# Kernel optimization log

Measured on AMD Instinct MI355X. Metric: run time of the kernel, lower is better.

Reference implementation:

```python
import jax, jax.numpy as jnp
import numpy as np
from jax import lax

BOS = 0
B, T, U = 8, 256, 64
IN, ENC_H, DEC_H, P, J, V = 80, 512, 512, 512, 512, 1024


def lstm_layer(x, Wih, Whh, b):
    """PyTorch-style LSTM layer. x: [B,T,I]; Wih: [4H,I]; Whh: [4H,H]; b: [4H]."""
    Bn = x.shape[0]
    H = Whh.shape[1]
    xp = jnp.einsum('bti,gi->btg', x, Wih) + b  # precompute input projections [B,T,4H]
    h0 = jnp.zeros((Bn, H), x.dtype)

    def step(carry, xt):
        h, c = carry
        g = xt + h @ Whh.T
        i, f, gg, o = jnp.split(g, 4, axis=-1)
        c = jax.nn.sigmoid(f) * c + jax.nn.sigmoid(i) * jnp.tanh(gg)
        h = jax.nn.sigmoid(o) * jnp.tanh(c)
        return (h, c), h

    _, hs = lax.scan(step, (h0, h0), xp.transpose(1, 0, 2))
    return hs.transpose(1, 0, 2)  # [B,T,H]


def setup_inputs() -> dict:
    key = jax.random.key(0)
    ks = jax.random.split(key, 20)
    s = 0.04  # ~1/sqrt(H) init scale
    inp = {
        'xs': jax.random.normal(ks[0], (B, T, IN), jnp.float32),
        'ys': jax.random.randint(ks[1], (B, U), 0, V),
        # encoder LSTM layer 0 / 1
        'enc_Wih0': jax.random.normal(ks[2], (4 * ENC_H, IN), jnp.float32) * s,
        'enc_Whh0': jax.random.normal(ks[3], (4 * ENC_H, ENC_H), jnp.float32) * s,
        'enc_b0': jnp.zeros((4 * ENC_H,), jnp.float32),
        'enc_Wih1': jax.random.normal(ks[4], (4 * ENC_H, ENC_H), jnp.float32) * s,
        'enc_Whh1': jax.random.normal(ks[5], (4 * ENC_H, ENC_H), jnp.float32) * s,
        'enc_b1': jnp.zeros((4 * ENC_H,), jnp.float32),
        'enc_projW': jax.random.normal(ks[6], (P, ENC_H), jnp.float32) * s,
        'enc_projb': jnp.zeros((P,), jnp.float32),
        # decoder
        'embed': jax.random.normal(ks[7], (V, DEC_H), jnp.float32) * s,
        'dec_Wih': jax.random.normal(ks[8], (4 * DEC_H, DEC_H), jnp.float32) * s,
        'dec_Whh': jax.random.normal(ks[9], (4 * DEC_H, DEC_H), jnp.float32) * s,
        'dec_b': jnp.zeros((4 * DEC_H,), jnp.float32),
        'dec_projW': jax.random.normal(ks[10], (P, DEC_H), jnp.float32) * s,
        'dec_projb': jnp.zeros((P,), jnp.float32),
        # joint MLP: Linear(2P -> J), Tanh, Linear(J -> V)
        'jW1': jax.random.normal(ks[11], (J, 2 * P), jnp.float32) * s,
        'jb1': jnp.zeros((J,), jnp.float32),
        'jW2': jax.random.normal(ks[12], (V, J), jnp.float32) * s,
        'jb2': jnp.zeros((V,), jnp.float32),
    }
    return inp


def reference(xs, ys, enc_Wih0, enc_Whh0, enc_b0, enc_Wih1, enc_Whh1, enc_b1,
              enc_projW, enc_projb, embed, dec_Wih, dec_Whh, dec_b,
              dec_projW, dec_projb, jW1, jb1, jW2, jb2):
    # Encoder: 2-layer LSTM + projection
    h = lstm_layer(xs, enc_Wih0, enc_Whh0, enc_b0)
    h = lstm_layer(h, enc_Wih1, enc_Whh1, enc_b1)
    h_enc = h @ enc_projW.T + enc_projb  # [B,T,P]

    # Decoder: BOS pad, embed, 1-layer LSTM + projection
    ys_p = jnp.pad(ys, ((0, 0), (1, 0)), constant_values=BOS)  # [B,U+1]
    e = embed[ys_p]
    hd = lstm_layer(e, dec_Wih, dec_Whh, dec_b)
    h_dec = hd @ dec_projW.T + dec_projb  # [B,U+1,P]

    # Joint: cat([h_enc,h_dec]) @ W1.T == h_enc @ W1[:,:P].T + h_dec @ W1[:,P:].T
    pre_enc = jnp.einsum('btp,jp->btj', h_enc, jW1[:, :P])
    pre_dec = jnp.einsum('bup,jp->buj', h_dec, jW1[:, P:])
    z = jnp.tanh(pre_enc[:, :, None, :] + pre_dec[:, None, :, :] + jb1)  # [B,T,U+1,J]
    logits = jnp.einsum('btuj,vj->btuv', z, jW2) + jb2  # [B,T,U+1,V]
    return logits
```

## Files before the change

### kernel.cpp

```cpp
#include <hip/hip_runtime.h>


typedef _Float16 f16;
typedef _Float16 f16x8 __attribute__((ext_vector_type(8)));
typedef float f32x4 __attribute__((ext_vector_type(4)));
using u32 = unsigned int;

#define BB   8
#define TT   256
#define UU1  65
#define HH   512
#define G4   2048
#define PP   512
#define JJ   512
#define VV   1024
#define SENT 0xFFFFFFFFu

#define LOADX(p)     __hip_atomic_load((p), __ATOMIC_RELAXED, __HIP_MEMORY_SCOPE_AGENT)
#define STOREX(p, v) __hip_atomic_store((p), (v), __ATOMIC_RELAXED, __HIP_MEMORY_SCOPE_AGENT)

static __device__ __forceinline__ u32 packf16(float a, float b) {
  f16 ha = (f16)a, hb = (f16)b;
  unsigned short ua = __builtin_bit_cast(unsigned short, ha);
  unsigned short ub = __builtin_bit_cast(unsigned short, hb);
  return (u32)ua | ((u32)ub << 16);
}
static __device__ __forceinline__ float sigm(float x) {
  x = fminf(30.f, fmaxf(-30.f, x));
  return __builtin_amdgcn_rcpf(1.f + __expf(-x));
}
static __device__ __forceinline__ float ftanh(float x) {
  x = fminf(15.f, fmaxf(-15.f, x));
  float t = __expf(2.f * x);
  return (t - 1.f) * __builtin_amdgcn_rcpf(t + 1.f);
}

__global__ void k_init(u32* __restrict__ p, int n, int z1, int z2) {
  int i = blockIdx.x * 256 + threadIdx.x;
  if (i >= n) return;
  bool z = (i < 2048) | ((u32)(i - z1) < 2048u) | ((u32)(i - z2) < 2048u);
  p[i] = z ? 0u : SENT;
}

struct CastSeg { const float* s; f16* d; int n4; };
struct CastArgs { CastSeg seg[10]; };
__global__ void k_cast_all(CastArgs a, int total4) {
  int i = blockIdx.x * 256 + threadIdx.x;
  if (i >= total4) return;
  int k = 0, off = i;
  while (off >= a.seg[k].n4) { off -= a.seg[k].n4; ++k; }
  const float4 v = *(const float4*)(a.seg[k].s + (size_t)off * 4);
  uint2 p; p.x = packf16(v.x, v.y); p.y = packf16(v.z, v.w);
  *(uint2*)(a.seg[k].d + (size_t)off * 4) = p;
}

__global__ void k_embed(const int* __restrict__ ys, const float* __restrict__ emb,
                        float* __restrict__ e) {
  int row = blockIdx.x;
  int b = row / UU1, u = row % UU1;
  int idx = (u == 0) ? 0 : ys[b * (UU1 - 1) + (u - 1)];
  const float4* s = (const float4*)(emb + (size_t)idx * HH);
  float4* d = (float4*)(e + (size_t)row * HH);
  d[threadIdx.x] = s[threadIdx.x];
}

__global__ void k_biasdot(const float* __restrict__ jW1, const float* __restrict__ encPb,
                          const float* __restrict__ dPb, const float* __restrict__ jb1,
                          float* __restrict__ bce, float* __restrict__ bcd) {
  int j = blockIdx.x * 256 + threadIdx.x;
  if (j >= 512) return;
  const float* rowE = jW1 + (size_t)j * 1024;
  const float* rowD = rowE + 512;
  float s1 = 0.f, s2 = 0.f;
  for (int p = 0; p < 512; p += 4) {
    float4 a = *(const float4*)(rowE + p), b = *(const float4*)(encPb + p);
    s1 += a.x * b.x + a.y * b.y + a.z * b.z + a.w * b.w;
    float4 c = *(const float4*)(rowD + p), d = *(const float4*)(dPb + p);
    s2 += c.x * d.x + c.y * d.y + c.z * d.z + c.w * d.w;
  }
  bce[j] = s1; bcd[j] = s2 + jb1[j];
}

__global__ __launch_bounds__(256) void k_gemm(
    const float* __restrict__ A, const f16* __restrict__ B,
    const float* __restrict__ bias, float* __restrict__ C,
    int M, int N, int K, int lda, int ldb) {
  __shared__ f16 As[128][72];
  __shared__ f16 Bs[128][72];
  int tid = threadIdx.x;
  int mb = blockIdx.y * 128, nb = blockIdx.x * 128;
  int wave = tid >> 6, lane = tid & 63;
  int wm = wave >> 1, wn = wave & 1;
  int rowa = lane & 15, kg = lane >> 4;
  f32x4 acc[4][4] = {};
  for (int k0 = 0; k0 < K; k0 += 64) {
    for (int idx = tid; idx < 2048; idx += 256) {
      int r = idx >> 4, cq = idx & 15;
      int gm = mb + r, gk = k0 + cq * 4;
      float4 v = make_float4(0.f, 0.f, 0.f, 0.f);
      if (gm < M && gk + 3 < K) v = *(const float4*)(A + (size_t)gm * lda + gk);
      uint2 p; p.x = packf16(v.x, v.y); p.y = packf16(v.z, v.w);
      *(uint2*)&As[r][cq * 4] = p;
    }
    for (int idx = tid; idx < 1024; idx += 256) {
      int r = idx >> 3, c8 = idx & 7;
      int gn = nb + r, gk = k0 + c8 * 8;
      uint4 v = make_uint4(0u, 0u, 0u, 0u);
      if (gn < N && gk + 7 < K) v = *(const uint4*)(B + (size_t)gn * ldb + gk);
      *(uint4*)&Bs[r][c8 * 8] = v;
    }
    __syncthreads();
#pragma unroll
    for (int kf = 0; kf < 2; ++kf) {
      f16x8 af[4], bf[4];
#pragma unroll
      for (int mt = 0; mt < 4; ++mt)
        af[mt] = *(const f16x8*)&As[wm * 64 + mt * 16 + rowa][kf * 32 + kg * 8];
#pragma unroll
      for (int nt = 0; nt < 4; ++nt)
        bf[nt] = *(const f16x8*)&Bs[wn * 64 + nt * 16 + rowa][kf * 32 + kg * 8];
#pragma unroll
      for (int mt = 0; mt < 4; ++mt)
#pragma unroll
        for (int nt = 0; nt < 4; ++nt)
          acc[mt][nt] = __builtin_amdgcn_mfma_f32_16x16x32_f16(af[mt], bf[nt], acc[mt][nt], 0, 0, 0);
    }
    __syncthreads();
  }
#pragma unroll
  for (int nt = 0; nt < 4; ++nt) {
    int gn = nb + wn * 64 + nt * 16 + rowa;
    float bv = bias ? bias[gn] : 0.f;
#pragma unroll
    for (int mt = 0; mt < 4; ++mt)
#pragma unroll
      for (int r = 0; r < 4; ++r) {
        int gm = mb + wm * 64 + mt * 16 + kg * 4 + r;
        if (gm < M) C[(size_t)gm * N + gn] = acc[mt][nt][r] + bv;
      }
  }
}

__global__ __launch_bounds__(256) void k_gemmT(
    const float* __restrict__ A, int lda, const f16* __restrict__ B2,
    f16* __restrict__ C16) {
  __shared__ f16 As[128][72];
  __shared__ f16 Bs[128][72];
  int tid = threadIdx.x;
  int mb = blockIdx.y * 128, nb = blockIdx.x * 128;
  int wave = tid >> 6, lane = tid & 63;
  int wm = wave >> 1, wn = wave & 1;
  int rowa = lane & 15, kg = lane >> 4;
  f32x4 acc[4][4] = {};
  for (int k0 = 0; k0 < 512; k0 += 64) {
    for (int idx = tid; idx < 2048; idx += 256) {
      int r = idx >> 4, cq = idx & 15;
      float4 v = *(const float4*)(A + (size_t)(mb + r) * lda + k0 + cq * 4);
      uint2 p; p.x = packf16(v.x, v.y); p.y = packf16(v.z, v.w);
      *(uint2*)&As[r][cq * 4] = p;
    }
    for (int idx = tid; idx < 1024; idx += 256) {
      int r = idx >> 4, c8 = idx & 15;
      uint4 v = *(const uint4*)(B2 + (size_t)(k0 + r) * 512 + nb + c8 * 8);
      f16 tmp[8]; *(uint4*)tmp = v;
#pragma unroll
      for (int e = 0; e < 8; ++e) Bs[c8 * 8 + e][r] = tmp[e];
    }
    __syncthreads();
#pragma unroll
    for (int kf = 0; kf < 2; ++kf) {
      f16x8 af[4], bf[4];
#pragma unroll
      for (int mt = 0; mt < 4; ++mt)
        af[mt] = *(const f16x8*)&As[wm * 64 + mt * 16 + rowa][kf * 32 + kg * 8];
#pragma unroll
      for (int nt = 0; nt < 4; ++nt)
        bf[nt] = *(const f16x8*)&Bs[wn * 64 + nt * 16 + rowa][kf * 32 + kg * 8];
#pragma unroll
      for (int mt = 0; mt < 4; ++mt)
#pragma unroll
        for (int nt = 0; nt < 4; ++nt)
          acc[mt][nt] = __builtin_amdgcn_mfma_f32_16x16x32_f16(af[mt], bf[nt], acc[mt][nt], 0, 0, 0);
    }
    __syncthreads();
  }
#pragma unroll
  for (int nt = 0; nt < 4; ++nt) {
    int gn = nb + wn * 64 + nt * 16 + rowa;
#pragma unroll
    for (int mt = 0; mt < 4; ++mt)
#pragma unroll
      for (int r = 0; r < 4; ++r) {
        int gm = mb + wm * 64 + mt * 16 + kg * 4 + r;
        C16[(size_t)gm * 512 + gn] = (f16)acc[mt][nt][r];
      }
  }
}

template <int NW>
static __device__ __forceinline__ void poll_batch(const u32* const* p, u32* vv) {
#pragma unroll
  for (int k = 0; k < NW; ++k) vv[k] = LOADX(p[k]);
  int gd = 0;
  while (++gd < (1 << 18)) {
    bool any = false;
#pragma unroll
    for (int k = 0; k < NW; ++k) any = any | (vv[k] == SENT);
    if (!any) break;
    __builtin_amdgcn_s_sleep(4);
#pragma unroll
    for (int k = 0; k < NW; ++k)
      if (vv[k] == SENT) vv[k] = LOADX(p[k]);
  }
}
static __device__ __forceinline__ void guard_spin(const u32* gp) {
  u32 v = LOADX(gp);
  int gd = 0;
  while (v == SENT && ++gd < (1 << 18)) {
    __builtin_amdgcn_s_sleep(1);
    v = LOADX(gp);
  }
}

static __device__ __forceinline__ void lstm_16(
    int wg, const float* __restrict__ xp, const f16* __restrict__ Whh,
    u32* __restrict__ hseq,
    float* __restrict__ hs, int S) {
  extern __shared__ char smem[];
  f16 (*W)[520] = (f16(*)[520])smem;
  f16 (*H)[520] = (f16(*)[520])(smem + 133120);
  float (*gat)[8][36] = (float(*)[8][36])(smem + 133120 + 8320);
  const int tid = threadIdx.x;
  const int u0 = wg * 32;
  const int wave = tid >> 6, lane = tid & 63;
  const int rowa = lane & 15, kg = lane >> 4;
  const int b = lane >> 3, ju = lane & 7;
  const int uglob = u0 + wave * 8 + ju;

  for (int idx = tid; idx < 128 * 64; idx += 256) {
    int r = idx >> 6, ck = idx & 63;
    int w = r >> 5, g = (r >> 3) & 3, u = r & 7;
    uint4 v = *(const uint4*)(Whh + ((size_t)(g * 512 + u0 + w * 8 + u)) * 512 + ck * 8);
    *(uint4*)&W[r][ck * 8] = v;
  }
  __syncthreads();

  float c = 0.f;
  for (int t = 0; t < S; ++t) {
    const u32* hb = hseq + (size_t)t * 2048;
    if (tid < 16) guard_spin(hb + tid * 16);
    __syncthreads();

    size_t xpo = ((size_t)b * S + t) * (size_t)G4 + uglob;
    float xi = xp[xpo], xf = xp[xpo + 512], xg = xp[xpo + 1024], xo = xp[xpo + 1536];

    const u32* ptr[8];
    u32 vv[8];
#pragma unroll
    for (int k = 0; k < 8; ++k) ptr[k] = hb + ((tid + k * 256) >> 8) * 256 + ((tid + k * 256) & 255);
    poll_batch<8>(ptr, vv);
#pragma unroll
    for (int k = 0; k < 8; ++k) {
      int idx = tid + k * 256;
      ((u32*)H)[(idx >> 8) * 260 + (idx & 255)] = vv[k];
    }
    __syncthreads();

    f32x4 acc0 = {0.f, 0.f, 0.f, 0.f}, acc1 = {0.f, 0.f, 0.f, 0.f};
#pragma unroll
    for (int kf = 0; kf < 16; ++kf) {
      f16x8 af = {};
      if (rowa < 8) af = *(const f16x8*)&H[rowa][kf * 32 + kg * 8];
      f16x8 b0 = *(const f16x8*)&W[wave * 32 + rowa][kf * 32 + kg * 8];
      f16x8 b1 = *(const f16x8*)&W[wave * 32 + 16 + rowa][kf * 32 + kg * 8];
      acc0 = __builtin_amdgcn_mfma_f32_16x16x32_f16(af, b0, acc0, 0, 0, 0);
      acc1 = __builtin_amdgcn_mfma_f32_16x16x32_f16(af, b1, acc1, 0, 0, 0);
    }
    if (kg < 2) {
#pragma unroll
      for (int r = 0; r < 4; ++r) {
        gat[wave][kg * 4 + r][rowa] = acc0[r];
        gat[wave][kg * 4 + r][16 + rowa] = acc1[r];
      }
    }
    float gi = gat[wave][b][ju] + xi;
    float gf = gat[wave][b][8 + ju] + xf;
    float gg = gat[wave][b][16 + ju] + xg;
    float go = gat[wave][b][24 + ju] + xo;
    c = sigm(gf) * c + sigm(gi) * ftanh(gg);
    float h = sigm(go) * ftanh(c);

    float hn = __shfl_down(h, 1);
    if ((ju & 1) == 0)
      STOREX(hseq + (size_t)(t + 1) * 2048 + ((b * 512 + uglob) >> 1), packf16(h, hn));
    if (hs) hs[((size_t)b * S + t) * HH + uglob] = h;
  }
}

static __device__ __forceinline__ void lstm_l1(
    int wg, const float* __restrict__ gb, const f16* __restrict__ Wih,
    const f16* __restrict__ Whh, const u32* __restrict__ hin,
    u32* __restrict__ hseq, float* __restrict__ hs, int S) {
  extern __shared__ char smem[];
  f16 (*W)[1032] = (f16(*)[1032])smem;
  f16 (*H)[1032] = (f16(*)[1032])(smem + 132096);
  float (*gat)[8][20] = (float(*)[8][20])(smem + 132096 + 16512);
  const int tid = threadIdx.x;
  const int u0 = wg * 16;
  const int wave = tid >> 6, lane = tid & 63;
  const int rowa = lane & 15, kg = lane >> 4;
  const int b = lane >> 2, ju = lane & 3;
  const int uglob = u0 + wave * 4 + ju;

  for (int idx = tid; idx < 64 * 64; idx += 256) {
    int r = idx >> 6, ck = idx & 63;
    int w = r >> 4, g = (r >> 2) & 3, u = r & 3;
    size_t grow = (size_t)(g * 512 + u0 + w * 4 + u) * 512;
    *(uint4*)&W[r][ck * 8]       = *(const uint4*)(Whh + grow + ck * 8);
    *(uint4*)&W[r][512 + ck * 8] = *(const uint4*)(Wih + grow + ck * 8);
  }
  float gbi = 0.f, gbf = 0.f, gbg = 0.f, gbo = 0.f;
  if (lane < 32) {
    gbi = gb[uglob]; gbf = gb[512 + uglob];
    gbg = gb[1024 + uglob]; gbo = gb[1536 + uglob];
  }
  __syncthreads();

  float c = 0.f;
  for (int t = 0; t < S; ++t) {
    const u32* hbS = hseq + (size_t)t * 2048;
    const u32* hbU = hin + (size_t)(t + 1) * 2048;
    if (tid < 32)       guard_spin(hbS + tid * 8);
    else if (tid < 48)  guard_spin(hbU + (tid - 32) * 16);
    __syncthreads();
    const u32* ptr[16];
    u32 vv[16];
#pragma unroll
    for (int k = 0; k < 8; ++k) {
      int idx = tid + k * 256;
      int r = idx >> 8, cu = idx & 255;
      ptr[k] = hbS + r * 256 + cu;
      ptr[k + 8] = hbU + r * 256 + cu;
    }
    poll_batch<16>(ptr, vv);
#pragma unroll
    for (int k = 0; k < 8; ++k) {
      int idx = tid + k * 256;
      int r = idx >> 8, cu = idx & 255;
      ((u32*)H)[r * 516 + cu] = vv[k];
      ((u32*)H)[r * 516 + 256 + cu] = vv[k + 8];
    }
    __syncthreads();

    f32x4 accA = {0.f, 0.f, 0.f, 0.f}, accB = {0.f, 0.f, 0.f, 0.f};
#pragma unroll
    for (int kf = 0; kf < 16; ++kf) {
      f16x8 afA = {}, afB = {};
      if (rowa < 8) {
        afA = *(const f16x8*)&H[rowa][kf * 32 + kg * 8];
        afB = *(const f16x8*)&H[rowa][(kf + 16) * 32 + kg * 8];
      }
      f16x8 bfA = *(const f16x8*)&W[wave * 16 + rowa][kf * 32 + kg * 8];
      f16x8 bfB = *(const f16x8*)&W[wave * 16 + rowa][(kf + 16) * 32 + kg * 8];
      accA = __builtin_amdgcn_mfma_f32_16x16x32_f16(afA, bfA, accA, 0, 0, 0);
      accB = __builtin_amdgcn_mfma_f32_16x16x32_f16(afB, bfB, accB, 0, 0, 0);
    }
    if (kg < 2) {
#pragma unroll
      for (int r = 0; r < 4; ++r) gat[wave][kg * 4 + r][rowa] = accA[r] + accB[r];
    }
    if (lane < 32) {
      float gi = gat[wave][b][ju]      + gbi;
      float gf = gat[wave][b][4 + ju]  + gbf;
      float gg = gat[wave][b][8 + ju]  + gbg;
      float go = gat[wave][b][12 + ju] + gbo;
      c = sigm(gf) * c + sigm(gi) * ftanh(gg);
      float h = sigm(go) * ftanh(c);
      float hn = __shfl_down(h, 1);
      if ((ju & 1) == 0)
        STOREX(hseq + (size_t)(t + 1) * 2048 + (b * 256 + (uglob >> 1)), packf16(h, hn));
      hs[((size_t)b * S + t) * HH + uglob] = h;
    }
  }
}

__global__ __launch_bounds__(256, 1) void k_lstm3(
    const float* xp0, const f16* Whh0, u32* hseq0,
    const float* b1, const f16* Wih1, const f16* Whh1, u32* hseq1, float* h1s,
    const float* xpd, const f16* Whhd, u32* hseqD, float* hds) {
  int g = blockIdx.x;
  if (g < 16)      lstm_16(g, xp0, Whh0, hseq0, nullptr, TT);
  else if (g < 48) lstm_l1(g - 16, b1, Wih1, Whh1, hseq0, hseq1, h1s, TT);
  else             lstm_16(g - 48, xpd, Whhd, hseqD, hds, UU1);
}

__global__ __launch_bounds__(512, 6) void k_joint(
    const float* __restrict__ pre_enc,
    const float* __restrict__ pre_dec,
    const f16* __restrict__ jW2,
    const float* __restrict__ jb2,
    float* __restrict__ out) {
  __shared__ f16 Z[32][520];
  __shared__ f16 Bs[64][72];
  __shared__ float Cs[32][68];
  int tid = threadIdx.x;
  int m0 = blockIdx.x * 32;
  const int wave = tid >> 6, lane = tid & 63;
  const int mt = wave >> 2, vt = wave & 3;
  const int rowa = lane & 15, kg = lane >> 4;
  const int r8 = tid >> 3, c8 = tid & 7;

  uint4 nreg = *(const uint4*)(jW2 + (size_t)r8 * JJ + c8 * 8);

  {
    int r = tid >> 4, q = tid & 15;
    int m = m0 + r;
    int bb = m / (TT * UU1);
    int rem = m % (TT * UU1);
    int t = rem / UU1, u = rem % UU1;
    const float* pe = pre_enc + ((size_t)bb * TT + t) * JJ + q * 32;
    const float* pd = pre_dec + ((size_t)bb * UU1 + u) * JJ + q * 32;
    for (int i = 0; i < 32; i += 8) {
      float4 e0 = *(const float4*)(pe + i);
      float4 e1 = *(const float4*)(pe + i + 4);
      float4 d0 = *(const float4*)(pd + i);
      float4 d1 = *(const float4*)(pd + i + 4);
      float z0 = ftanh(e0.x + d0.x), z1 = ftanh(e0.y + d0.y);
      float z2 = ftanh(e0.z + d0.z), z3 = ftanh(e0.w + d0.w);
      float z4 = ftanh(e1.x + d1.x), z5 = ftanh(e1.y + d1.y);
      float z6 = ftanh(e1.z + d1.z), z7 = ftanh(e1.w + d1.w);
      uint4 p; p.x = packf16(z0, z1); p.y = packf16(z2, z3);
      p.z = packf16(z4, z5); p.w = packf16(z6, z7);
      *(uint4*)&Z[r][q * 32 + i] = p;
    }
  }

  f32x4 acc = {};
  for (int it = 0; it < 128; ++it) {
    const int vc = it >> 3, ks = it & 7;
    __syncthreads();
    *(uint4*)&Bs[r8][c8 * 8] = nreg;
    if (it < 127) {
      int nvc = (it + 1) >> 3, nks = (it + 1) & 7;
      nreg = *(const uint4*)(jW2 + (size_t)(nvc * 64 + r8) * JJ + nks * 64 + c8 * 8);
    }
    __syncthreads();
#pragma unroll
    for (int kf = 0; kf < 2; ++kf) {
      f16x8 af = *(const f16x8*)&Bs[vt * 16 + rowa][kf * 32 + kg * 8];
      f16x8 bf = *(const f16x8*)&Z[mt * 16 + rowa][ks * 64 + kf * 32 + kg * 8];
      acc = __builtin_amdgcn_mfma_f32_16x16x32_f16(af, bf, acc, 0, 0, 0);
    }
    if (ks == 7) {
      int vl = vt * 16 + kg * 4;
      float4 bv = *(const float4*)(jb2 + vc * 64 + vl);
      f32x4 st;
      st[0] = acc[0] + bv.x; st[1] = acc[1] + bv.y;
      st[2] = acc[2] + bv.z; st[3] = acc[3] + bv.w;
      *(f32x4*)&Cs[mt * 16 + rowa][vl] = st;
      acc = (f32x4){0.f, 0.f, 0.f, 0.f};
      __syncthreads();
      int m = tid >> 4, vi = (tid & 15) * 4;
      f32x4 row = *(const f32x4*)&Cs[m][vi];
      __builtin_nontemporal_store(row,
          (f32x4*)(out + (size_t)(m0 + m) * VV + vc * 64 + vi));
    }
  }
}

extern "C" void kernel_launch(void* const* d_in, const int* in_sizes, int n_in,
                              void* d_out, int out_size, void* d_ws, size_t ws_size,
                              hipStream_t stream) {
  const float* xs    = (const float*)d_in[0];
  const int*   ys    = (const int*)d_in[1];
  const float* Wih0  = (const float*)d_in[2];
  const float* Whh0  = (const float*)d_in[3];
  const float* b0    = (const float*)d_in[4];
  const float* Wih1  = (const float*)d_in[5];
  const float* Whh1  = (const float*)d_in[6];
  const float* b1    = (const float*)d_in[7];
  const float* encPW = (const float*)d_in[8];
  const float* encPb = (const float*)d_in[9];
  const float* embed = (const float*)d_in[10];
  const float* dWih  = (const float*)d_in[11];
  const float* dWhh  = (const float*)d_in[12];
  const float* db    = (const float*)d_in[13];
  const float* dPW   = (const float*)d_in[14];
  const float* dPb   = (const float*)d_in[15];
  const float* jW1   = (const float*)d_in[16];
  const float* jb1   = (const float*)d_in[17];
  const float* jW2   = (const float*)d_in[18];
  const float* jb2   = (const float*)d_in[19];
  float* out = (float*)d_out;

  char* base = (char*)d_ws;
  size_t off = 0;
  auto alc = [&](size_t bytes) -> char* {
    char* p = base + off;
    off = (off + bytes + 255) & ~(size_t)255;
    return p;
  };
  f16* Wih0h = (f16*)alc((size_t)2048 * 80 * 2);
  f16* Whh0h = (f16*)alc((size_t)2048 * 512 * 2);
  f16* Wih1h = (f16*)alc((size_t)2048 * 512 * 2);
  f16* Whh1h = (f16*)alc((size_t)2048 * 512 * 2);
  f16* dWihh = (f16*)alc((size_t)2048 * 512 * 2);
  f16* dWhhh = (f16*)alc((size_t)2048 * 512 * 2);
  f16* ePWh  = (f16*)alc((size_t)512 * 512 * 2);
  f16* dPWh  = (f16*)alc((size_t)512 * 512 * 2);
  f16* jW2h  = (f16*)alc((size_t)1024 * 512 * 2);
  f16* Wceh  = (f16*)alc((size_t)512 * 512 * 2);
  f16* Wcdh  = (f16*)alc((size_t)512 * 512 * 2);
  float* bce  = (float*)alc((size_t)512 * 4);
  float* bcd  = (float*)alc((size_t)512 * 4);
  float* e    = (float*)alc((size_t)520 * 512 * 4);
  float* xp0  = (float*)alc((size_t)2048 * 2048 * 4);
  float* xpd  = (float*)alc((size_t)520 * 2048 * 4);
  float* h1s  = (float*)alc((size_t)2048 * 512 * 4);
  float* hds  = (float*)alc((size_t)520 * 512 * 4);
  float* penc = (float*)alc((size_t)2048 * 512 * 4);
  float* pdec = (float*)alc((size_t)520 * 512 * 4);
  u32* hseq0 = (u32*)alc((size_t)(TT + 1) * 2048 * 4);
  u32* hseq1 = (u32*)alc((size_t)(TT + 1) * 2048 * 4);
  u32* hseqD = (u32*)alc((size_t)(UU1 + 1) * 2048 * 4);
  if (off > ws_size) return;

  {
    int n = (int)(((TT + 1) * 2 + (UU1 + 1)) * 2048);
    int z1 = (int)(hseq1 - hseq0), z2 = (int)(hseqD - hseq0);
    k_init<<<dim3((n + 255) / 256), dim3(256), 0, stream>>>(hseq0, n, z1, z2);
  }
  {
    CastArgs ca = {};
    auto seg = [&](int i, const float* s, f16* d, size_t n) {
      ca.seg[i].s = s; ca.seg[i].d = d; ca.seg[i].n4 = (int)(n / 4);
    };
    seg(0, Wih0, Wih0h, (size_t)2048 * 80);
    seg(1, Whh0, Whh0h, (size_t)2048 * 512);
    seg(2, Wih1, Wih1h, (size_t)2048 * 512);
    seg(3, Whh1, Whh1h, (size_t)2048 * 512);
    seg(4, dWih, dWihh, (size_t)2048 * 512);
    seg(5, dWhh, dWhhh, (size_t)2048 * 512);
    seg(6, encPW, ePWh, (size_t)512 * 512);
    seg(7, dPW, dPWh, (size_t)512 * 512);
    seg(8, jW2, jW2h, (size_t)1024 * 512);
    int total4 = 0;
    for (int i = 0; i < 9; ++i) total4 += ca.seg[i].n4;
    k_cast_all<<<dim3((total4 + 255) / 256), dim3(256), 0, stream>>>(ca, total4);
  }
  k_gemmT<<<dim3(4, 4), dim3(256), 0, stream>>>(jW1, 1024, ePWh, Wceh);
  k_gemmT<<<dim3(4, 4), dim3(256), 0, stream>>>(jW1 + 512, 1024, dPWh, Wcdh);
  k_biasdot<<<dim3(2), dim3(256), 0, stream>>>(jW1, encPb, dPb, jb1, bce, bcd);

  k_embed<<<dim3(520), dim3(128), 0, stream>>>(ys, embed, e);

  auto gemm = [&](const float* A, const f16* B, const float* bias, float* C,
                  int M, int N, int K, int lda, int ldb) {
    k_gemm<<<dim3(N / 128, (M + 127) / 128), dim3(256), 0, stream>>>(
        A, B, bias, C, M, N, K, lda, ldb);
  };

  gemm(xs, Wih0h, b0, xp0, 2048, 2048, 80, 80, 80);
  gemm(e, dWihh, db, xpd, 520, 2048, 512, 512, 512);

  k_lstm3<<<dim3(64), dim3(256), 151168, stream>>>(
      xp0, Whh0h, hseq0,
      b1, Wih1h, Whh1h, hseq1, h1s,
      xpd, dWhhh, hseqD, hds);

  gemm(h1s, Wceh, bce, penc, 2048, 512, 512, 512, 512);
  gemm(hds, Wcdh, bcd, pdec, 520, 512, 512, 512, 512);

  k_joint<<<dim3(4160), dim3(512), 0, stream>>>(penc, pdec, jW2h, jb2, out);
}
```

Baseline: 1.428 ms.

## Fuse projections and joint into persistent LSTM kernel with flag-based streaming

```diff
diff --git a/kernel.cpp b/kernel.cpp
--- a/kernel.cpp
+++ b/kernel.cpp
@@ -11,7 +11,6 @@
 #define UU1  65
 #define HH   512
 #define G4   2048
-#define PP   512
 #define JJ   512
 #define VV   1024
 #define SENT 0xFFFFFFFFu
@@ -224,8 +223,7 @@
 
 static __device__ __forceinline__ void lstm_16(
     int wg, const float* __restrict__ xp, const f16* __restrict__ Whh,
-    u32* __restrict__ hseq,
-    float* __restrict__ hs, int S) {
+    u32* __restrict__ hseq, int S) {
   extern __shared__ char smem[];
   f16 (*W)[520] = (f16(*)[520])smem;
   f16 (*H)[520] = (f16(*)[520])(smem + 133120);
@@ -293,14 +291,13 @@
     float hn = __shfl_down(h, 1);
     if ((ju & 1) == 0)
       STOREX(hseq + (size_t)(t + 1) * 2048 + ((b * 512 + uglob) >> 1), packf16(h, hn));
-    if (hs) hs[((size_t)b * S + t) * HH + uglob] = h;
   }
 }
 
 static __device__ __forceinline__ void lstm_l1(
     int wg, const float* __restrict__ gb, const f16* __restrict__ Wih,
     const f16* __restrict__ Whh, const u32* __restrict__ hin,
-    u32* __restrict__ hseq, float* __restrict__ hs, int S) {
+    u32* __restrict__ hseq, int S) {
   extern __shared__ char smem[];
   f16 (*W)[1032] = (f16(*)[1032])smem;
   f16 (*H)[1032] = (f16(*)[1032])(smem + 132096);
@@ -379,93 +376,178 @@
       float hn = __shfl_down(h, 1);
       if ((ju & 1) == 0)
         STOREX(hseq + (size_t)(t + 1) * 2048 + (b * 256 + (uglob >> 1)), packf16(h, hn));
-      hs[((size_t)b * S + t) * HH + uglob] = h;
-    }
-  }
-}
-
-__global__ __launch_bounds__(256, 1) void k_lstm3(
-    const float* xp0, const f16* Whh0, u32* hseq0,
-    const float* b1, const f16* Wih1, const f16* Whh1, u32* hseq1, float* h1s,
-    const float* xpd, const f16* Whhd, u32* hseqD, float* hds) {
-  int g = blockIdx.x;
-  if (g < 16)      lstm_16(g, xp0, Whh0, hseq0, nullptr, TT);
-  else if (g < 48) lstm_l1(g - 16, b1, Wih1, Whh1, hseq0, hseq1, h1s, TT);
-  else             lstm_16(g - 48, xpd, Whhd, hseqD, hds, UU1);
-}
-
-__global__ __launch_bounds__(512, 6) void k_joint(
-    const float* __restrict__ pre_enc,
-    const float* __restrict__ pre_dec,
-    const f16* __restrict__ jW2,
-    const float* __restrict__ jb2,
+    }
+  }
+}
+
+static __device__ __forceinline__ void proj_prod(
+    int wg, const u32* __restrict__ hseq, const f16* __restrict__ Wc,
+    const float* __restrict__ bc, float* __restrict__ outS, int S,
+    int gs, int gc) {
+  extern __shared__ char smem[];
+  f16 (*W)[520] = (f16(*)[520])smem;
+  f16 (*H)[520] = (f16(*)[520])(smem + 66560);
+  const int tid = threadIdx.x;
+  const int wave = tid >> 6, lane = tid & 63;
+  const int rowa = lane & 15, kg = lane >> 4;
+  const int c0 = wg * 64;
+  const int j = c0 + wave * 16 + rowa;
+
+  for (int idx = tid; idx < 64 * 64; idx += 256) {
+    int r = idx >> 6, ck = idx & 63;
+    uint4 v = *(const uint4*)(Wc + (size_t)(c0 + r) * 512 + ck * 8);
+    *(uint4*)&W[r][ck * 8] = v;
+  }
+  for (int idx = tid; idx < 16 * 260; idx += 256) ((u32*)H)[idx] = 0u;
+  const float bj = bc[j];
+  __syncthreads();
+
+  for (int t = 0; t < S; ++t) {
+    const u32* hb = hseq + (size_t)(t + 1) * 2048;
+    if (tid < gc) guard_spin(hb + tid * gs);
+    __syncthreads();
+    const u32* ptr[8];
+    u32 vv[8];
+#pragma unroll
+    for (int k = 0; k < 8; ++k) ptr[k] = hb + ((tid + k * 256) >> 8) * 256 + ((tid + k * 256) & 255);
+    poll_batch<8>(ptr, vv);
+#pragma unroll
+    for (int k = 0; k < 8; ++k) {
+      int idx = tid + k * 256;
+      ((u32*)H)[(idx >> 8) * 260 + (idx & 255)] = vv[k];
+    }
+    __syncthreads();
+
+    f32x4 acc = {0.f, 0.f, 0.f, 0.f};
+#pragma unroll
+    for (int kf = 0; kf < 16; ++kf) {
+      f16x8 af = {};
+      if (rowa < 8) af = *(const f16x8*)&H[rowa][kf * 32 + kg * 8];
+      f16x8 bf = *(const f16x8*)&W[wave * 16 + rowa][kf * 32 + kg * 8];
+      acc = __builtin_amdgcn_mfma_f32_16x16x32_f16(af, bf, acc, 0, 0, 0);
+    }
+    if (kg < 2) {
+#pragma unroll
+      for (int r = 0; r < 4; ++r) {
+        float val = acc[r] + bj;
+        STOREX((u32*)(outS + ((size_t)t * 8 + kg * 4 + r) * 512 + j),
+               __builtin_bit_cast(u32, val));
+      }
+    }
+  }
+}
+
+static __device__ __forceinline__ void joint_tile(
+    int j, const float* __restrict__ pencS, const float* __restrict__ pdecS,
+    const f16* __restrict__ jW2, const float* __restrict__ jb2,
     float* __restrict__ out) {
-  __shared__ f16 Z[32][520];
-  __shared__ f16 Bs[64][72];
-  __shared__ float Cs[32][68];
-  int tid = threadIdx.x;
-  int m0 = blockIdx.x * 32;
+  extern __shared__ char smem[];
+  f16 (*Z)[520] = (f16(*)[520])smem;
+  f16 (*Bs)[72] = (f16(*)[72])(smem + 49920);
+  float (*Cs)[68] = (float(*)[68])(smem + 49920 + 9216);
+  const int tid = threadIdx.x;
+  const int t = j >> 4, b = (j >> 1) & 7, uh = j & 1;
+  const int u0 = uh * 32, nrow = uh ? 33 : 32;
+  const size_t mbase = (size_t)b * (TT * UU1) + (size_t)t * UU1 + u0;
   const int wave = tid >> 6, lane = tid & 63;
-  const int mt = wave >> 2, vt = wave & 3;
   const int rowa = lane & 15, kg = lane >> 4;
-  const int r8 = tid >> 3, c8 = tid & 7;
-
-  uint4 nreg = *(const uint4*)(jW2 + (size_t)r8 * JJ + c8 * 8);
-
+
+  const int rr = tid >> 2, cc = (tid & 3) * 16;
+  uint4 n0 = *(const uint4*)(jW2 + (size_t)rr * JJ + cc);
+  uint4 n1 = *(const uint4*)(jW2 + (size_t)rr * JJ + cc + 8);
+
+  for (int idx = tid; idx < 48 * 260; idx += 256) ((u32*)Z)[idx] = 0u;
   {
-    int r = tid >> 4, q = tid & 15;
-    int m = m0 + r;
-    int bb = m / (TT * UU1);
-    int rem = m % (TT * UU1);
-    int t = rem / UU1, u = rem % UU1;
-    const float* pe = pre_enc + ((size_t)bb * TT + t) * JJ + q * 32;
-    const float* pd = pre_dec + ((size_t)bb * UU1 + u) * JJ + q * 32;
-    for (int i = 0; i < 32; i += 8) {
-      float4 e0 = *(const float4*)(pe + i);
-      float4 e1 = *(const float4*)(pe + i + 4);
-      float4 d0 = *(const float4*)(pd + i);
-      float4 d1 = *(const float4*)(pd + i + 4);
-      float z0 = ftanh(e0.x + d0.x), z1 = ftanh(e0.y + d0.y);
-      float z2 = ftanh(e0.z + d0.z), z3 = ftanh(e0.w + d0.w);
-      float z4 = ftanh(e1.x + d1.x), z5 = ftanh(e1.y + d1.y);
-      float z6 = ftanh(e1.z + d1.z), z7 = ftanh(e1.w + d1.w);
-      uint4 p; p.x = packf16(z0, z1); p.y = packf16(z2, z3);
-      p.z = packf16(z4, z5); p.w = packf16(z6, z7);
-      *(uint4*)&Z[r][q * 32 + i] = p;
-    }
-  }
-
-  f32x4 acc = {};
+    const u32* pe = (const u32*)(pencS + ((size_t)t * 8 + b) * 512);
+    for (int r = tid >> 4; r < nrow; r += 16) {
+      const u32* pd = (const u32*)(pdecS + ((size_t)(u0 + r) * 8 + b) * 512);
+      int cbase = (tid & 15) * 32;
+      for (int c8 = 0; c8 < 4; ++c8) {
+        const u32* ptr[8];
+        u32 ve[8], vd[8];
+#pragma unroll
+        for (int k = 0; k < 8; ++k) ptr[k] = pe + cbase + c8 * 8 + k;
+        poll_batch<8>(ptr, ve);
+#pragma unroll
+        for (int k = 0; k < 8; ++k) ptr[k] = pd + cbase + c8 * 8 + k;
+        poll_batch<8>(ptr, vd);
+        uint4 p;
+        float z0 = ftanh(__builtin_bit_cast(float, ve[0]) + __builtin_bit_cast(float, vd[0]));
+        float z1 = ftanh(__builtin_bit_cast(float, ve[1]) + __builtin_bit_cast(float, vd[1]));
+        float z2 = ftanh(__builtin_bit_cast(float, ve[2]) + __builtin_bit_cast(float, vd[2]));
+        float z3 = ftanh(__builtin_bit_cast(float, ve[3]) + __builtin_bit_cast(float, vd[3]));
+        float z4 = ftanh(__builtin_bit_cast(float, ve[4]) + __builtin_bit_cast(float, vd[4]));
+        float z5 = ftanh(__builtin_bit_cast(float, ve[5]) + __builtin_bit_cast(float, vd[5]));
+        float z6 = ftanh(__builtin_bit_cast(float, ve[6]) + __builtin_bit_cast(float, vd[6]));
+        float z7 = ftanh(__builtin_bit_cast(float, ve[7]) + __builtin_bit_cast(float, vd[7]));
+        p.x = packf16(z0, z1); p.y = packf16(z2, z3);
+        p.z = packf16(z4, z5); p.w = packf16(z6, z7);
+        *(uint4*)&Z[r][cbase + c8 * 8] = p;
+      }
+    }
+  }
+
+  f32x4 acc[3] = {};
   for (int it = 0; it < 128; ++it) {
     const int vc = it >> 3, ks = it & 7;
     __syncthreads();
-    *(uint4*)&Bs[r8][c8 * 8] = nreg;
+    *(uint4*)&Bs[rr][cc] = n0;
+    *(uint4*)&Bs[rr][cc + 8] = n1;
     if (it < 127) {
       int nvc = (it + 1) >> 3, nks = (it + 1) & 7;
-      nreg = *(const uint4*)(jW2 + (size_t)(nvc * 64 + r8) * JJ + nks * 64 + c8 * 8);
+      const f16* p = jW2 + (size_t)(nvc * 64 + rr) * JJ + nks * 64 + cc;
+      n0 = *(const uint4*)p;
+      n1 = *(const uint4*)(p + 8);
     }
     __syncthreads();
 #pragma unroll
     for (int kf = 0; kf < 2; ++kf) {
-      f16x8 af = *(const f16x8*)&Bs[vt * 16 + rowa][kf * 32 + kg * 8];
-      f16x8 bf = *(const f16x8*)&Z[mt * 16 + rowa][ks * 64 + kf * 32 + kg * 8];
-      acc = __builtin_amdgcn_mfma_f32_16x16x32_f16(af, bf, acc, 0, 0, 0);
+      f16x8 af = *(const f16x8*)&Bs[wave * 16 + rowa][kf * 32 + kg * 8];
+#pragma unroll
+      for (int mt = 0; mt < 3; ++mt) {
+        f16x8 bf = *(const f16x8*)&Z[mt * 16 + rowa][ks * 64 + kf * 32 + kg * 8];
+        acc[mt] = __builtin_amdgcn_mfma_f32_16x16x32_f16(af, bf, acc[mt], 0, 0, 0);
+      }
     }
     if (ks == 7) {
-      int vl = vt * 16 + kg * 4;
+      int vl = wave * 16 + kg * 4;
       float4 bv = *(const float4*)(jb2 + vc * 64 + vl);
-      f32x4 st;
-      st[0] = acc[0] + bv.x; st[1] = acc[1] + bv.y;
-      st[2] = acc[2] + bv.z; st[3] = acc[3] + bv.w;
-      *(f32x4*)&Cs[mt * 16 + rowa][vl] = st;
-      acc = (f32x4){0.f, 0.f, 0.f, 0.f};
+#pragma unroll
+      for (int mt = 0; mt < 3; ++mt) {
+        int row = mt * 16 + rowa;
+        if (row < nrow) {
+          f32x4 st;
+          st[0] = acc[mt][0] + bv.x; st[1] = acc[mt][1] + bv.y;
+          st[2] = acc[mt][2] + bv.z; st[3] = acc[mt][3] + bv.w;
+          *(f32x4*)&Cs[row][vl] = st;
+        }
+        acc[mt] = (f32x4){0.f, 0.f, 0.f, 0.f};
+      }
       __syncthreads();
-      int m = tid >> 4, vi = (tid & 15) * 4;
-      f32x4 row = *(const f32x4*)&Cs[m][vi];
-      __builtin_nontemporal_store(row,
-          (f32x4*)(out + (size_t)(m0 + m) * VV + vc * 64 + vi));
-    }
-  }
+      for (int r = tid >> 4; r < nrow; r += 16) {
+        int vi = (tid & 15) * 4;
+        f32x4 rowv = *(const f32x4*)&Cs[r][vi];
+        __builtin_nontemporal_store(rowv,
+            (f32x4*)(out + (mbase + r) * VV + vc * 64 + vi));
+      }
+    }
+  }
+}
+
+__global__ __launch_bounds__(256, 1) void k_all(
+    const float* xp0, const f16* Whh0, u32* hseq0,
+    const float* b1, const f16* Wih1, const f16* Whh1, u32* hseq1,
+    const float* xpd, const f16* Whhd, u32* hseqD,
+    const f16* Wce, const float* bce, float* pencS,
+    const f16* Wcd, const float* bcd, float* pdecS,
+    const f16* jW2, const float* jb2, float* out) {
+  int g = blockIdx.x;
+  if (g < 16)       lstm_16(g, xp0, Whh0, hseq0, TT);
+  else if (g < 48)  lstm_l1(g - 16, b1, Wih1, Whh1, hseq0, hseq1, TT);
+  else if (g < 64)  lstm_16(g - 48, xpd, Whhd, hseqD, UU1);
+  else if (g < 72)  proj_prod(g - 64, hseq1, Wce, bce, pencS, TT, 8, 32);
+  else if (g < 80)  proj_prod(g - 72, hseqD, Wcd, bcd, pdecS, UU1, 16, 16);
+  else              joint_tile(g - 80, pencS, pdecS, jW2, jb2, out);
 }
 
 extern "C" void kernel_launch(void* const* d_in, const int* in_sizes, int n_in,
@@ -516,17 +598,15 @@
   float* e    = (float*)alc((size_t)520 * 512 * 4);
   float* xp0  = (float*)alc((size_t)2048 * 2048 * 4);
   float* xpd  = (float*)alc((size_t)520 * 2048 * 4);
-  float* h1s  = (float*)alc((size_t)2048 * 512 * 4);
-  float* hds  = (float*)alc((size_t)520 * 512 * 4);
-  float* penc = (float*)alc((size_t)2048 * 512 * 4);
-  float* pdec = (float*)alc((size_t)520 * 512 * 4);
   u32* hseq0 = (u32*)alc((size_t)(TT + 1) * 2048 * 4);
   u32* hseq1 = (u32*)alc((size_t)(TT + 1) * 2048 * 4);
   u32* hseqD = (u32*)alc((size_t)(UU1 + 1) * 2048 * 4);
+  float* pencS = (float*)alc((size_t)TT * 8 * 512 * 4);
+  float* pdecS = (float*)alc((size_t)UU1 * 8 * 512 * 4);
   if (off > ws_size) return;
 
   {
-    int n = (int)(((TT + 1) * 2 + (UU1 + 1)) * 2048);
+    int n = (int)(((TT + 1) * 2 + (UU1 + 1)) * 2048 + TT * 8 * 512 + UU1 * 8 * 512);
     int z1 = (int)(hseq1 - hseq0), z2 = (int)(hseqD - hseq0);
     k_init<<<dim3((n + 255) / 256), dim3(256), 0, stream>>>(hseq0, n, z1, z2);
   }
@@ -563,13 +643,11 @@
   gemm(xs, Wih0h, b0, xp0, 2048, 2048, 80, 80, 80);
   gemm(e, dWihh, db, xpd, 520, 2048, 512, 512, 512);
 
-  k_lstm3<<<dim3(64), dim3(256), 151168, stream>>>(
+  k_all<<<dim3(80 + 4096), dim3(256), 151168, stream>>>(
       xp0, Whh0h, hseq0,
-      b1, Wih1h, Whh1h, hseq1, h1s,
-      xpd, dWhhh, hseqD, hds);
-
-  gemm(h1s, Wceh, bce, penc, 2048, 512, 512, 512, 512);
-  gemm(hds, Wcdh, bcd, pdec, 520, 512, 512, 512, 512);
-
-  k_joint<<<dim3(4160), dim3(512), 0, stream>>>(penc, pdec, jW2h, jb2, out);
-}
+      b1, Wih1h, Whh1h, hseq1,
+      xpd, dWhhh, hseqD,
+      Wceh, bce, pencS,
+      Wcdh, bcd, pdecS,
+      jW2h, jb2, out);
+}
```

Measured after the change: 1.699 ms. +18.9%, slower.
